# Optimization experiments

Hardware: AMD Instinct MI355X
Metric: run time of the kernel (lower is better)

The kernel has to match this reference:

```python
import jax, jax.numpy as jnp
import numpy as np

B, H, E, D = 16384, 1024, 64, 128  # batch, hidden, nb_entities, wh_units==we_units


def setup_inputs() -> dict:
    key = jax.random.key(0)
    k0, k1, k2 = jax.random.split(key, 3)
    hidden_state = jax.random.normal(k0, (B, H), dtype=jnp.float32)
    # Wh: Dense(wh_units) acting on H -> D
    Wh_w = jax.random.normal(k1, (H, D), dtype=jnp.float32) * 0.02
    Wh_b = jnp.zeros((D,), dtype=jnp.float32)
    # We: nb_entities separate Dense(we_units), stacked into one [E, D, D] tensor
    We_w = jax.random.normal(k2, (E, D, D), dtype=jnp.float32) * 0.02
    We_b = jnp.zeros((E, D), dtype=jnp.float32)
    return {"hidden_state": hidden_state, "Wh_w": Wh_w, "Wh_b": Wh_b,
            "We_w": We_w, "We_b": We_b}


def reference(hidden_state, Wh_w, Wh_b, We_w, We_b):
    # reduced_dimentionality = Wh(hidden_state)            [B, D]
    r = hidden_state @ Wh_w + Wh_b
    # per-entity Dense loop + concat + transpose == one batched GEMM -> [B, E, D]
    logits = jnp.einsum('bk,ekd->bed', r, We_w) + We_b[None, :, :]
    outputs = jax.nn.softmax(logits, axis=-1)               # [B, E, D]
    # second pass: We[i] applied to outputs[:, i, :]       [B, E, D]
    vt = jnp.einsum('bek,ekd->bed', outputs, We_w) + We_b[None, :, :]
    # transpose to [B, D, E] then reduce_sum over E == sum over entity axis
    result = vt.sum(axis=1)                                 # [B, D]
    return (outputs, result)
```

## Files before the change

### kernel.cpp

```cpp
#include <hip/hip_runtime.h>
#include <hip/hip_bf16.h>

typedef __attribute__((ext_vector_type(8))) short short8;
typedef __attribute__((ext_vector_type(4))) float f32x4;
typedef __attribute__((ext_vector_type(4))) unsigned int uint4v;
typedef __attribute__((ext_vector_type(2))) unsigned int uint2v;

#define NB 16384
#define NH 1024
#define NE 64
#define ND 128
#define BR 32
#define GRP 4

static __device__ __forceinline__ unsigned short f2b(float x) {
  unsigned int u = __builtin_bit_cast(unsigned int, x);
  unsigned int r = (u + 0x7fffu + ((u >> 16) & 1u)) >> 16;
  return (unsigned short)r;
}
static __device__ __forceinline__ float b2f_lo(unsigned int u) {
  return __builtin_bit_cast(float, u << 16);
}
static __device__ __forceinline__ float b2f_hi(unsigned int u) {
  return __builtin_bit_cast(float, u & 0xffff0000u);
}

static __device__ __forceinline__ void bar_sync() {
  __builtin_amdgcn_sched_barrier(0);
  asm volatile("s_waitcnt lgkmcnt(0)" ::: "memory");
  __builtin_amdgcn_sched_barrier(0);
  __builtin_amdgcn_s_barrier();
  __builtin_amdgcn_sched_barrier(0);
}

static __device__ __forceinline__ int swz(int row, int col) {
  return (row << 7) + ((((col >> 3) ^ (row & 15)) << 3) | (col & 7));
}
static __device__ __forceinline__ int pswz(int row, int eg, int col) {
  return ((row * GRP + eg) << 7) + ((((col >> 3) ^ (row & 15)) << 3) | (col & 7));
}

__global__ __launch_bounds__(256, 1) void k0_prep(
    const float* __restrict__ Wh_w, const float* __restrict__ We_w,
    const float* __restrict__ We_b,
    unsigned short* __restrict__ WeT, unsigned short* __restrict__ WhT,
    float* __restrict__ bsum)
{
  __shared__ float tile[32][33];
  const int bid = blockIdx.x, t = threadIdx.x;
  const int i = t >> 5, j = t & 31;
  if (bid < 1024) {
    const int e = bid >> 4, tr = (bid >> 2) & 3, tc = bid & 3;
    const float* src = We_w + (size_t)e * 16384;
#pragma unroll
    for (int k = 0; k < 4; ++k)
      tile[i + 8 * k][j] = src[(size_t)(tr * 32 + i + 8 * k) * 128 + tc * 32 + j];
    __syncthreads();
    unsigned short* dst = WeT + (size_t)e * 16384;
#pragma unroll
    for (int k = 0; k < 4; ++k) {
      int row = i + 8 * k;
      dst[(size_t)(tc * 32 + row) * 128 + tr * 32 + j] = f2b(tile[j][row]);
    }
  } else if (bid < 1152) {
    const int tb = bid - 1024, tr = tb >> 2, tc = tb & 3;
#pragma unroll
    for (int k = 0; k < 4; ++k)
      tile[i + 8 * k][j] = Wh_w[(size_t)(tr * 32 + i + 8 * k) * 128 + tc * 32 + j];
    __syncthreads();
#pragma unroll
    for (int k = 0; k < 4; ++k) {
      int row = i + 8 * k;
      WhT[(size_t)(tc * 32 + row) * 1024 + tr * 32 + j] = f2b(tile[j][row]);
    }
  } else {
    if (t < 128) {
      float s = 0.f;
      for (int e = 0; e < 64; ++e) s += We_b[e * 128 + t];
      bsum[t] = s;
    }
  }
}

__global__ __launch_bounds__(256, 2) void k1_rgemm(
    const float* __restrict__ hidden, const unsigned short* __restrict__ WhT,
    const float* __restrict__ Wh_b, unsigned short* __restrict__ r_g)
{
  const int t = threadIdx.x;
  const int w = t >> 6, l = t & 63, c = l & 15, g = l >> 4;
  const int bg = w & 1, dh = w >> 1;
  const int b = blockIdx.x * 32 + 16 * bg + c;
  const float* hrow = hidden + (size_t)b * NH;
  f32x4 acc[4];
#pragma unroll
  for (int mf = 0; mf < 4; ++mf) acc[mf] = (f32x4){0.f, 0.f, 0.f, 0.f};
#pragma unroll 2
  for (int ks = 0; ks < 32; ++ks) {
    const int k0 = 8 * g + 32 * ks;
    f32x4 h0 = *(const f32x4*)(hrow + k0);
    f32x4 h1 = *(const f32x4*)(hrow + k0 + 4);
    short8 bf;
    bf[0] = (short)f2b(h0[0]); bf[1] = (short)f2b(h0[1]);
    bf[2] = (short)f2b(h0[2]); bf[3] = (short)f2b(h0[3]);
    bf[4] = (short)f2b(h1[0]); bf[5] = (short)f2b(h1[1]);
    bf[6] = (short)f2b(h1[2]); bf[7] = (short)f2b(h1[3]);
#pragma unroll
    for (int mf = 0; mf < 4; ++mf) {
      short8 af = *(const short8*)(WhT + (size_t)(64 * dh + 16 * mf + c) * NH + k0);
      acc[mf] = __builtin_amdgcn_mfma_f32_16x16x32_bf16(af, bf, acc[mf], 0, 0, 0);
    }
  }
#pragma unroll
  for (int mf = 0; mf < 4; ++mf) {
    const int d0 = 64 * dh + 16 * mf + 4 * g;
    f32x4 bias = *(const f32x4*)(Wh_b + d0);
    f32x4 v = acc[mf] + bias;
    unsigned int lo = (unsigned)f2b(v[0]) | ((unsigned)f2b(v[1]) << 16);
    unsigned int hi = (unsigned)f2b(v[2]) | ((unsigned)f2b(v[3]) << 16);
    uint2v pk = {lo, hi};
    *(uint2v*)(r_g + (size_t)b * ND + d0) = pk;
  }
}

struct SmemK2 {
  union {
    unsigned short Pst[BR * GRP * 128];
    float obuf[BR * 128];
  };
  unsigned short r_lds[BR * 128];
  float sms[4][BR];
};

static __device__ __forceinline__ void load_we_frags(
    short8 (&f)[2][4], f32x4 (&bias)[2],
    const unsigned short* __restrict__ WeT, const float* __restrict__ We_b,
    int e, int w, int c, int g)
{
  const unsigned short* base = WeT + (size_t)e * (ND * ND);
#pragma unroll
  for (int mf = 0; mf < 2; ++mf) {
    const unsigned short* rowp = base + (size_t)(16 * (2 * w + mf) + c) * ND + 8 * g;
#pragma unroll
    for (int ks = 0; ks < 4; ++ks)
      f[mf][ks] = *(const short8*)(rowp + 32 * ks);
    bias[mf] = *(const f32x4*)(We_b + e * ND + 32 * w + 16 * mf + 4 * g);
  }
}

static __device__ __forceinline__ void store_p_slice(
    const SmemK2& sm, float* __restrict__ outP,
    int brow0, int e_prev, int slice, int t)
{
#pragma unroll
  for (int it = 0; it < 4; ++it) {
    const int flat = it * 1024 + t * 4;
    const int row = flat >> 7;
    const int col = flat & 127;
    uint2v u = *(const uint2v*)(&sm.Pst[pswz(row, slice, col)]);
    f32x4 v;
    v[0] = b2f_lo(u[0]); v[1] = b2f_hi(u[0]);
    v[2] = b2f_lo(u[1]); v[3] = b2f_hi(u[1]);
    float* dst = outP + ((size_t)(brow0 + row) * NE + e_prev) * ND + col;
    __builtin_nontemporal_store(v, (f32x4*)dst);
  }
}

static __device__ __forceinline__ void entity_body(
    int i, int en, int e_prev, bool do_store,
    int brow0, int w, int c, int g, int t,
    short8 (&cur)[2][4], short8 (&nxt)[2][4],
    f32x4 (&bcur)[2], f32x4 (&bnxt)[2], f32x4 (&acc2)[2][2],
    const unsigned short* __restrict__ WeT, const float* __restrict__ We_b,
    float* __restrict__ outP, SmemK2& sm)
{
  const int eg = i & 3, pg = (i + 3) & 3;
  f32x4 acc1[2][2];
#pragma unroll
  for (int mf = 0; mf < 2; ++mf)
#pragma unroll
    for (int nf = 0; nf < 2; ++nf) acc1[mf][nf] = (f32x4){0.f, 0.f, 0.f, 0.f};
#pragma unroll
  for (int ks = 0; ks < 4; ++ks) {
    short8 b1[2];
#pragma unroll
    for (int nf = 0; nf < 2; ++nf)
      b1[nf] = *(const short8*)(&sm.r_lds[swz(16 * nf + c, 8 * g + 32 * ks)]);
#pragma unroll
    for (int mf = 0; mf < 2; ++mf)
#pragma unroll
      for (int nf = 0; nf < 2; ++nf)
        acc1[mf][nf] = __builtin_amdgcn_mfma_f32_16x16x32_bf16(
            cur[mf][ks], b1[nf], acc1[mf][nf], 0, 0, 0);
  }
  load_we_frags(nxt, bnxt, WeT, We_b, en, w, c, g);
  __builtin_amdgcn_sched_barrier(0);
  if (do_store) store_p_slice(sm, outP, brow0, e_prev, pg, t);

#pragma unroll
  for (int mf = 0; mf < 2; ++mf)
#pragma unroll
    for (int nf = 0; nf < 2; ++nf) acc1[mf][nf] += bcur[mf];
  float s[2] = {0.f, 0.f};
#pragma unroll
  for (int nf = 0; nf < 2; ++nf) {
#pragma unroll
    for (int mf = 0; mf < 2; ++mf)
#pragma unroll
      for (int r = 0; r < 4; ++r) {
        float p = __expf(acc1[mf][nf][r]);
        acc1[mf][nf][r] = p;
        s[nf] += p;
      }
    s[nf] += __shfl_xor(s[nf], 16);
    s[nf] += __shfl_xor(s[nf], 32);
  }
  if (g == 0) {
#pragma unroll
    for (int nf = 0; nf < 2; ++nf) sm.sms[w][16 * nf + c] = s[nf];
  }
  bar_sync();
  float inv[2];
#pragma unroll
  for (int nf = 0; nf < 2; ++nf) {
    int b = 16 * nf + c;
    inv[nf] = 1.f / (sm.sms[0][b] + sm.sms[1][b] + sm.sms[2][b] + sm.sms[3][b]);
  }
#pragma unroll
  for (int mf = 0; mf < 2; ++mf)
#pragma unroll
    for (int nf = 0; nf < 2; ++nf) {
      f32x4 p = acc1[mf][nf] * inv[nf];
      unsigned int lo = (unsigned)f2b(p[0]) | ((unsigned)f2b(p[1]) << 16);
      unsigned int hi = (unsigned)f2b(p[2]) | ((unsigned)f2b(p[3]) << 16);
      uint2v pk = {lo, hi};
      *(uint2v*)(&sm.Pst[pswz(16 * nf + c, eg, 32 * w + 16 * mf + 4 * g)]) = pk;
    }
  bar_sync();

#pragma unroll
  for (int ks = 0; ks < 4; ++ks) {
    short8 a2[2];
#pragma unroll
    for (int mf2 = 0; mf2 < 2; ++mf2)
      a2[mf2] = *(const short8*)(&sm.Pst[pswz(16 * mf2 + c, eg, 8 * g + 32 * ks)]);
#pragma unroll
    for (int mf2 = 0; mf2 < 2; ++mf2)
#pragma unroll
      for (int n = 0; n < 2; ++n)
        acc2[mf2][n] = __builtin_amdgcn_mfma_f32_16x16x32_bf16(
            a2[mf2], cur[n][ks], acc2[mf2][n], 0, 0, 0);
  }
}

__global__ __launch_bounds__(256, 2) void k2_main(
    const unsigned short* __restrict__ r_g, const unsigned short* __restrict__ WeT,
    const float* __restrict__ We_b, const float* __restrict__ bsum,
    float* __restrict__ outP, float* __restrict__ outR)
{
  __shared__ SmemK2 sm;
  const int t = threadIdx.x;
  const int w = t >> 6, l = t & 63, c = l & 15, g = l >> 4;
  const int lb = (blockIdx.x & 7) * 64 + (blockIdx.x >> 3);
  const int brow0 = lb * BR;
  const int e0 = (((lb >> 6) + lb) & 7) << 3;

  for (int i = t; i < BR * 16; i += 256) {
    int row = i >> 4, ch = i & 15;
    uint4v v = *(const uint4v*)(r_g + (size_t)(brow0 + row) * ND + ch * 8);
    *(uint4v*)(&sm.r_lds[swz(row, ch * 8)]) = v;
  }
  const float bs0 = bsum[32 * w + c];
  const float bs1 = bsum[32 * w + 16 + c];

  f32x4 acc2[2][2];
#pragma unroll
  for (int i = 0; i < 2; ++i)
#pragma unroll
    for (int j = 0; j < 2; ++j) acc2[i][j] = (f32x4){0.f, 0.f, 0.f, 0.f};

  short8 wa[2][4], wb[2][4];
  f32x4 ba[2], bb[2];
  load_we_frags(wa, ba, WeT, We_b, e0, w, c, g);
  bar_sync();

#pragma unroll 1
  for (int i = 0; i < NE; i += 2) {
    const int eB = (e0 + i + 1) & 63, eC = (e0 + i + 2) & 63;
    const int pA = (e0 + i + 63) & 63, pB = (e0 + i) & 63;
    entity_body(i,     eB, pA, i > 0, brow0, w, c, g, t,
                wa, wb, ba, bb, acc2, WeT, We_b, outP, sm);
    entity_body(i + 1, eC, pB, true,  brow0, w, c, g, t,
                wb, wa, bb, ba, acc2, WeT, We_b, outP, sm);
  }
  store_p_slice(sm, outP, brow0, (e0 + 63) & 63, 3, t);

  bar_sync();
#pragma unroll
  for (int mf2 = 0; mf2 < 2; ++mf2)
#pragma unroll
    for (int n = 0; n < 2; ++n) {
      float bs = n ? bs1 : bs0;
#pragma unroll
      for (int r = 0; r < 4; ++r)
        sm.obuf[(16 * mf2 + 4 * g + r) * ND + 32 * w + 16 * n + c] =
            acc2[mf2][n][r] + bs;
    }
  bar_sync();
  {
    const int orow = t >> 5, ocol = (t & 31) * 4;
#pragma unroll
    for (int it = 0; it < 4; ++it) {
      const int row = orow + 8 * it;
      f32x4 v = *(const f32x4*)(&sm.obuf[row * ND + ocol]);
      __builtin_nontemporal_store(
          v, (f32x4*)(outR + (size_t)(brow0 + row) * ND + ocol));
    }
  }
}

extern "C" void kernel_launch(void* const* d_in, const int* in_sizes, int n_in,
                              void* d_out, int out_size, void* d_ws, size_t ws_size,
                              hipStream_t stream)
{
  (void)in_sizes; (void)n_in; (void)out_size; (void)ws_size;
  const float* hidden = (const float*)d_in[0];
  const float* Wh_w   = (const float*)d_in[1];
  const float* Wh_b   = (const float*)d_in[2];
  const float* We_w   = (const float*)d_in[3];
  const float* We_b   = (const float*)d_in[4];
  float* outP = (float*)d_out;
  float* outR = outP + (size_t)NB * NE * ND;

  char* ws = (char*)d_ws;
  unsigned short* WeT = (unsigned short*)(ws);
  unsigned short* WhT = (unsigned short*)(ws + 2097152);
  unsigned short* r_g = (unsigned short*)(ws + 2097152 + 262144);
  float* bsum         = (float*)(ws + 2097152 + 262144 + 4194304);

  k0_prep<<<1153, 256, 0, stream>>>(Wh_w, We_w, We_b, WeT, WhT, bsum);
  k1_rgemm<<<512, 256, 0, stream>>>(hidden, WhT, Wh_b, r_g);
  k2_main<<<512, 256, 0, stream>>>(r_g, WeT, We_b, bsum, outP, outR);
}
```

Measured before the change: 223.0 us.

## Stagger per-wave softmax output stores and hoist next-entity weight prefetch

Each wave now writes its own 8-row quarter of a buffered softmax slice. Wave w trails the compute by w+1 entities, so global stores spread across iterations instead of all waves storing a whole slice in one burst. The next entity's weight-fragment load moves ahead of the first GEMM so it overlaps more compute. The per-block starting entity is also hashed as (lb*37)&63 to spread concurrent blocks over more entities. The deeper lag relies on the 4-slot ring buffer not being overwritten before the trailing wave has read it, and adds a short epilogue loop that drains the remaining quarters.

```diff
diff --git a/kernel.cpp b/kernel.cpp
--- a/kernel.cpp
+++ b/kernel.cpp
@@ -147,14 +147,14 @@
   }
 }
 
-static __device__ __forceinline__ void store_p_slice(
+static __device__ __forceinline__ void store_p_quarter(
     const SmemK2& sm, float* __restrict__ outP,
-    int brow0, int e_prev, int slice, int t)
+    int brow0, int e_prev, int slice, int w, int l)
 {
 #pragma unroll
   for (int it = 0; it < 4; ++it) {
-    const int flat = it * 1024 + t * 4;
-    const int row = flat >> 7;
+    const int flat = it * 256 + l * 4;
+    const int row = 8 * w + (flat >> 7);
     const int col = flat & 127;
     uint2v u = *(const uint2v*)(&sm.Pst[pswz(row, slice, col)]);
     f32x4 v;
@@ -166,14 +166,20 @@
 }
 
 static __device__ __forceinline__ void entity_body(
-    int i, int en, int e_prev, bool do_store,
-    int brow0, int w, int c, int g, int t,
+    int i, int en, int e0, int brow0, int w, int c, int g, int l,
     short8 (&cur)[2][4], short8 (&nxt)[2][4],
     f32x4 (&bcur)[2], f32x4 (&bnxt)[2], f32x4 (&acc2)[2][2],
     const unsigned short* __restrict__ WeT, const float* __restrict__ We_b,
     float* __restrict__ outP, SmemK2& sm)
 {
-  const int eg = i & 3, pg = (i + 3) & 3;
+  const int eg = i & 3;
+  load_we_frags(nxt, bnxt, WeT, We_b, en, w, c, g);
+  __builtin_amdgcn_sched_barrier(0);
+  if (i >= w + 1) {
+    const int j = i - 1 - w;
+    store_p_quarter(sm, outP, brow0, (e0 + j) & 63, j & 3, w, l);
+  }
+  __builtin_amdgcn_sched_barrier(0);
   f32x4 acc1[2][2];
 #pragma unroll
   for (int mf = 0; mf < 2; ++mf)
@@ -192,10 +198,6 @@
         acc1[mf][nf] = __builtin_amdgcn_mfma_f32_16x16x32_bf16(
             cur[mf][ks], b1[nf], acc1[mf][nf], 0, 0, 0);
   }
-  load_we_frags(nxt, bnxt, WeT, We_b, en, w, c, g);
-  __builtin_amdgcn_sched_barrier(0);
-  if (do_store) store_p_slice(sm, outP, brow0, e_prev, pg, t);
-
 #pragma unroll
   for (int mf = 0; mf < 2; ++mf)
 #pragma unroll
@@ -236,19 +238,18 @@
       *(uint2v*)(&sm.Pst[pswz(16 * nf + c, eg, 32 * w + 16 * mf + 4 * g)]) = pk;
     }
   bar_sync();
-
-#pragma unroll
-  for (int ks = 0; ks < 4; ++ks) {
+#pragma unroll
+  for (int ks2 = 0; ks2 < 4; ++ks2) {
     short8 a2[2];
 #pragma unroll
     for (int mf2 = 0; mf2 < 2; ++mf2)
-      a2[mf2] = *(const short8*)(&sm.Pst[pswz(16 * mf2 + c, eg, 8 * g + 32 * ks)]);
+      a2[mf2] = *(const short8*)(&sm.Pst[pswz(16 * mf2 + c, eg, 8 * g + 32 * ks2)]);
 #pragma unroll
     for (int mf2 = 0; mf2 < 2; ++mf2)
 #pragma unroll
       for (int n = 0; n < 2; ++n)
         acc2[mf2][n] = __builtin_amdgcn_mfma_f32_16x16x32_bf16(
-            a2[mf2], cur[n][ks], acc2[mf2][n], 0, 0, 0);
+            a2[mf2], cur[n][ks2], acc2[mf2][n], 0, 0, 0);
   }
 }
 
@@ -262,7 +263,7 @@
   const int w = t >> 6, l = t & 63, c = l & 15, g = l >> 4;
   const int lb = (blockIdx.x & 7) * 64 + (blockIdx.x >> 3);
   const int brow0 = lb * BR;
-  const int e0 = (((lb >> 6) + lb) & 7) << 3;
+  const int e0 = (lb * 37) & 63;
 
   for (int i = t; i < BR * 16; i += 256) {
     int row = i >> 4, ch = i & 15;
@@ -286,13 +287,13 @@
 #pragma unroll 1
   for (int i = 0; i < NE; i += 2) {
     const int eB = (e0 + i + 1) & 63, eC = (e0 + i + 2) & 63;
-    const int pA = (e0 + i + 63) & 63, pB = (e0 + i) & 63;
-    entity_body(i,     eB, pA, i > 0, brow0, w, c, g, t,
+    entity_body(i,     eB, e0, brow0, w, c, g, l,
                 wa, wb, ba, bb, acc2, WeT, We_b, outP, sm);
-    entity_body(i + 1, eC, pB, true,  brow0, w, c, g, t,
+    entity_body(i + 1, eC, e0, brow0, w, c, g, l,
                 wb, wa, bb, ba, acc2, WeT, We_b, outP, sm);
   }
-  store_p_slice(sm, outP, brow0, (e0 + 63) & 63, 3, t);
+  for (int j = 63 - w; j < 64; ++j)
+    store_p_quarter(sm, outP, brow0, (e0 + j) & 63, j & 3, w, l);
 
   bar_sync();
 #pragma unroll
```

After: 234.3 us. +5.1%, slower.
